# Kernel optimization log

Hardware: AMD Instinct MI355X
Metric: run time of the kernel (lower is better)

## Reference

```python
import jax, jax.numpy as jnp
import numpy as np
from functools import partial

EPS = 1e-6

def rmsnorm(x, w):
    rms = jnp.sqrt(jnp.mean(x * x, axis=-1, keepdims=True) + EPS)
    return x * w / rms

def causal_dwconv(x, w):
    # x: [B, T, D], w: [D, 1, k] depthwise kernel (torch Conv1d layout)
    D = x.shape[-1]
    k = w.shape[-1]
    xt = jnp.transpose(x, (0, 2, 1))  # [B, D, T]
    out = jax.lax.conv_general_dilated(
        xt, w, window_strides=(1,), padding=[(k - 1, 0)],
        dimension_numbers=("NCH", "OIH", "NCH"), feature_group_count=D)
    return jnp.transpose(out, (0, 2, 1))  # [B, T, D]

def setup_inputs() -> dict:
    key = jax.random.key(0)
    B, T, D, F, S = 2, 4096, 1024, 4096, 4096
    ks = jax.random.split(key, 20)
    s = 0.02
    return {
        "x": jax.random.normal(ks[0], (B, T, D), jnp.float32),
        "h_prev": jnp.zeros((B, D), jnp.float32),
        "norm1_w": jnp.ones((D,), jnp.float32),
        "conv3_w": jax.random.normal(ks[1], (D, 1, 3), jnp.float32) * s,
        "conv7_w": jax.random.normal(ks[2], (D, 1, 7), jnp.float32) * s,
        "conv15_w": jax.random.normal(ks[3], (D, 1, 15), jnp.float32) * s,
        "mix_w": jax.random.normal(ks[4], (D, D), jnp.float32) * s,
        "norm2_w": jnp.ones((D,), jnp.float32),
        "Wz_w": jax.random.normal(ks[5], (D, D), jnp.float32) * s,
        "Wz_b": jnp.zeros((D,), jnp.float32),
        "Wh_w": jax.random.normal(ks[6], (D, D), jnp.float32) * s,
        "Wh_b": jnp.zeros((D,), jnp.float32),
        "norm3_w": jnp.ones((D,), jnp.float32),
        "slot_keys": jax.random.normal(ks[7], (S, D), jnp.float32) * s,
        "slot_values": jax.random.normal(ks[8], (S, D), jnp.float32) * s,
        "projq_w": jax.random.normal(ks[9], (D, D), jnp.float32) * s,
        "projout_w": jax.random.normal(ks[10], (D, D), jnp.float32) * s,
        "norm4_w": jnp.ones((D,), jnp.float32),
        "gate_w": jax.random.normal(ks[11], (F, D), jnp.float32) * s,
        "up_w": jax.random.normal(ks[12], (F, D), jnp.float32) * s,
        "down_w": jax.random.normal(ks[13], (D, F), jnp.float32) * s,
    }

def resonance_forward(x, h_prev, norm1_w, conv3_w, conv7_w, conv15_w, mix_w,
                      norm2_w, Wz_w, Wz_b, Wh_w, Wh_b, norm3_w, slot_keys,
                      slot_values, projq_w, projout_w, norm4_w, gate_w, up_w, down_w):
    B, T, D = x.shape
    top_k = 2
    # 1. multi-scale causal conv block
    xn = rmsnorm(x, norm1_w)
    conv = causal_dwconv(xn, conv3_w) + causal_dwconv(xn, conv7_w) + causal_dwconv(xn, conv15_w)
    x = x + conv @ mix_w.T
    # 2. MinGRU: precompute gates, then linear recurrence via scan
    xn = rmsnorm(x, norm2_w)
    z = jax.nn.sigmoid(xn @ Wz_w.T + Wz_b)        # [B, T, D]
    h_tilde = xn @ Wh_w.T + Wh_b                  # [B, T, D]
    def step(h, zh):
        zt, ht = zh
        h = (1.0 - zt) * h + zt * ht
        return h, h
    h_last, hs = jax.lax.scan(step, h_prev,
                              (jnp.swapaxes(z, 0, 1), jnp.swapaxes(h_tilde, 0, 1)))
    x = x + jnp.swapaxes(hs, 0, 1)
    # 3. slot memory with top-k routing
    xn = rmsnorm(x, norm3_w)
    q = xn @ projq_w.T
    scores = (q @ slot_keys.T) / jnp.sqrt(jnp.asarray(D, x.dtype))  # [B, T, S]
    topk_vals, topk_ids = jax.lax.top_k(scores, top_k)              # [B, T, k]
    attn = jax.nn.softmax(topk_vals, axis=-1)
    gathered = slot_values[topk_ids]                                # [B, T, k, D]
    retrieved = jnp.einsum("btk,btkd->btd", attn, gathered)
    x = x + retrieved @ projout_w.T
    # 4. SwiGLU FFN
    xn = rmsnorm(x, norm4_w)
    ff = (jax.nn.silu(xn @ gate_w.T) * (xn @ up_w.T)) @ down_w.T
    x = x + ff
    return x, h_last

def reference(x, h_prev, norm1_w, conv3_w, conv7_w, conv15_w, mix_w, norm2_w,
              Wz_w, Wz_b, Wh_w, Wh_b, norm3_w, slot_keys, slot_values,
              projq_w, projout_w, norm4_w, gate_w, up_w, down_w):
    return resonance_forward(x, h_prev, norm1_w, conv3_w, conv7_w, conv15_w,
                             mix_w, norm2_w, Wz_w, Wz_b, Wh_w, Wh_b, norm3_w,
                             slot_keys, slot_values, projq_w, projout_w,
                             norm4_w, gate_w, up_w, down_w)
```

## Files before the change

### kernel.cpp

```cpp
#include <hip/hip_runtime.h>
#include <hip/hip_bf16.h>
#include <cstdint>

#define BB   2
#define TT   4096
#define DD   1024
#define FF   4096
#define SS   4096
#define MTOK (BB * TT)
#define NCHUNK 32
#define TCHUNK 128

typedef __bf16 bf16x8 __attribute__((ext_vector_type(8)));
typedef float  f32x4  __attribute__((ext_vector_type(4)));
typedef __attribute__((address_space(3))) char lds_char;
typedef __attribute__((address_space(1))) char g_char;

struct CvtArgs {
  const float* src[9];
  __hip_bfloat16* dst[9];
  int off4[10];
  int mode[9];
};

__global__ __launch_bounds__(256) void cvt_all_kernel(CvtArgs a) {
  int g = blockIdx.x * 256 + threadIdx.x;
  if (g >= a.off4[9]) return;
  int s = 0;
  while (g >= a.off4[s + 1]) s++;
  int i = g - a.off4[s];
  float4 v = ((const float4*)a.src[s])[i];
  union { ushort4 u; __hip_bfloat16 h[4]; } p;
  p.h[0] = __float2bfloat16(v.x);
  p.h[1] = __float2bfloat16(v.y);
  p.h[2] = __float2bfloat16(v.z);
  p.h[3] = __float2bfloat16(v.w);
  int di = i;
  int m = a.mode[s];
  if (m) {
    int r = i >> 8, c = i & 255;
    int dr = ((r >> 4) << 5) + (r & 15) + ((m == 2) ? 16 : 0);
    di = (dr << 8) + c;
  }
  ((ushort4*)a.dst[s])[di] = p.u;
}

__global__ void wcomb_kernel(const float* __restrict__ w3, const float* __restrict__ w7,
                             const float* __restrict__ w15, float* __restrict__ wc) {
  int d = blockIdx.x * 256 + threadIdx.x;
  if (d >= DD) return;
  for (int j = 0; j < 16; j++) {
    float v = 0.f;
    if (j < 15) {
      v = w15[d * 15 + (14 - j)];
      if (j < 7) v += w7[d * 7 + (6 - j)];
      if (j < 3) v += w3[d * 3 + (2 - j)];
    }
    wc[d * 16 + j] = v;
  }
}

__global__ __launch_bounds__(256) void rms_kernel(const float* __restrict__ x,
                                                  const float* __restrict__ w,
                                                  __hip_bfloat16* __restrict__ ob) {
  const int row = blockIdx.x;
  const int tid = threadIdx.x;
  float4 v = ((const float4*)(x + (size_t)row * DD))[tid];
  float ss = v.x * v.x + v.y * v.y + v.z * v.z + v.w * v.w;
  for (int off = 32; off > 0; off >>= 1) ss += __shfl_down(ss, off, 64);
  __shared__ float wsum[4];
  if ((tid & 63) == 0) wsum[tid >> 6] = ss;
  __syncthreads();
  float tot = wsum[0] + wsum[1] + wsum[2] + wsum[3];
  float rinv = 1.0f / sqrtf(tot * (1.0f / DD) + 1e-6f);
  float4 wg = ((const float4*)w)[tid];
  union { ushort4 u; __hip_bfloat16 h[4]; } p;
  p.h[0] = __float2bfloat16(v.x * wg.x * rinv);
  p.h[1] = __float2bfloat16(v.y * wg.y * rinv);
  p.h[2] = __float2bfloat16(v.z * wg.z * rinv);
  p.h[3] = __float2bfloat16(v.w * wg.w * rinv);
  ((ushort4*)ob)[(size_t)row * 256 + tid] = p.u;
}

__global__ __launch_bounds__(256) void conv_kernel(const __hip_bfloat16* __restrict__ xn,
                                                   const float* __restrict__ wc,
                                                   __hip_bfloat16* __restrict__ outp) {
  __shared__ float xt[78][64];
  __shared__ float wt[64][15];
  const int b = blockIdx.z, t0 = blockIdx.x * 64, d0 = blockIdx.y * 64;
  const int tid = threadIdx.x;
  const int dl = tid & 63;
  for (int idx = tid; idx < 64 * 15; idx += 256) {
    int d = idx / 15, j = idx % 15;
    wt[d][j] = wc[(d0 + d) * 16 + j];
  }
  for (int r = tid >> 6; r < 78; r += 4) {
    int t = t0 - 14 + r;
    xt[r][dl] = (t >= 0) ? __bfloat162float(xn[((size_t)b * TT + t) * DD + d0 + dl]) : 0.f;
  }
  __syncthreads();
  for (int tl = tid >> 6; tl < 64; tl += 4) {
    float acc = 0.f;
#pragma unroll
    for (int j = 0; j < 15; j++) acc += wt[dl][j] * xt[tl + 14 - j][dl];
    outp[((size_t)b * TT + t0 + tl) * DD + d0 + dl] = __float2bfloat16(acc);
  }
}

template <int EPI, int KSPLIT = 1>
__global__ __launch_bounds__(256, 2) void gemm_bt(
    const __hip_bfloat16* __restrict__ A, const __hip_bfloat16* __restrict__ Bm,
    const int M, const int N, const int K,
    float* __restrict__ outf, __hip_bfloat16* __restrict__ outb,
    const float* __restrict__ bias0, const float* __restrict__ bias1) {
  __shared__ __align__(16) __hip_bfloat16 As[128 * 32];
  __shared__ __align__(16) __hip_bfloat16 Bs[128 * 32];
  const int tid = threadIdx.x;
  const int lane = tid & 63;
  const int wave = tid >> 6;
  const int fm = lane & 15, fq = lane >> 4;

  const int nT = gridDim.x;
  const int lin = blockIdx.y * nT + blockIdx.x;
  const int xcd = lin & 7;
  const int idx_ = lin >> 3;
  const int mq = idx_ / nT;
  const int tileM = (xcd * (gridDim.y >> 3) + mq) * 128;
  const int tileN = (idx_ - mq * nT) * 128;

  const int wm = (wave & 1) * 64, wn = (wave >> 1) * 64;

  f32x4 acc[4][4] = {};

  const int srow = tid >> 2;
  const int scol = (tid & 3) * 8;
  const __hip_bfloat16* gA = A + (size_t)(tileM + srow) * K + scol;
  const __hip_bfloat16* gB = Bm + (size_t)(tileN + srow) * K + scol;
  lds_char* ldsA = (lds_char*)(&As[0]);
  lds_char* ldsB = (lds_char*)(&Bs[0]);
  const int wbyte = wave * 1024;

  const int kPer = K / KSPLIT;
  const int kBeg = (KSPLIT > 1) ? blockIdx.z * kPer : 0;
  for (int k0 = kBeg; k0 < kBeg + kPer; k0 += 32) {
    __syncthreads();
    __builtin_amdgcn_global_load_lds((g_char*)(void*)(gA + k0),                  ldsA + wbyte,        16, 0, 0);
    __builtin_amdgcn_global_load_lds((g_char*)(void*)(gA + k0 + (size_t)64 * K), ldsA + wbyte + 4096, 16, 0, 0);
    __builtin_amdgcn_global_load_lds((g_char*)(void*)(gB + k0),                  ldsB + wbyte,        16, 0, 0);
    __builtin_amdgcn_global_load_lds((g_char*)(void*)(gB + k0 + (size_t)64 * K), ldsB + wbyte + 4096, 16, 0, 0);
    __syncthreads();
    bf16x8 af[4], bfr[4];
#pragma unroll
    for (int i = 0; i < 4; i++) {
      af[i]  = *(const bf16x8*)(As + (wm + i * 16 + fm) * 32 + fq * 8);
      bfr[i] = *(const bf16x8*)(Bs + (wn + i * 16 + fm) * 32 + fq * 8);
    }
#pragma unroll
    for (int i = 0; i < 4; i++)
#pragma unroll
      for (int j = 0; j < 4; j++)
        acc[i][j] = __builtin_amdgcn_mfma_f32_16x16x32_bf16(af[i], bfr[j], acc[i][j], 0, 0, 0);
  }

  if constexpr (EPI == 7) {
#pragma unroll
    for (int i = 0; i < 4; i++) {
#pragma unroll
      for (int j = 0; j < 4; j += 2) {
        const int ffcol = (((tileN + wn + j * 16) >> 5) << 4) + fm;
#pragma unroll
        for (int r = 0; r < 4; r++) {
          const int rw = tileM + wm + i * 16 + fq * 4 + r;
          float g = acc[i][j][r];
          float u = acc[i][j + 1][r];
          float v = g / (1.f + __expf(-g)) * u;
          outb[(size_t)rw * FF + ffcol] = __float2bfloat16(v);
        }
      }
    }
  } else {
#pragma unroll
    for (int i = 0; i < 4; i++) {
#pragma unroll
      for (int j = 0; j < 4; j++) {
        const int c = tileN + wn + j * 16 + fm;
#pragma unroll
        for (int r = 0; r < 4; r++) {
          const int rw = tileM + wm + i * 16 + fq * 4 + r;
          const size_t idx = (size_t)rw * N + c;
          float v = acc[i][j][r];
          if constexpr (EPI == 1) {
            v += (c < DD) ? bias0[c] : bias1[c - DD];
            if (c < DD) v = 1.f / (1.f + __expf(-v));
            outb[idx] = __float2bfloat16(v);
          } else if constexpr (EPI == 2) {
            outb[idx] = __float2bfloat16(v);
          } else if constexpr (EPI == 6) {
            outf[(size_t)blockIdx.z * M * N + idx] = v;
          }
        }
      }
    }
  }
}

template <int EPI>
__global__ __launch_bounds__(256, 4) void gemm_bt64(
    const __hip_bfloat16* __restrict__ A, const __hip_bfloat16* __restrict__ Bm,
    const int M, const int N, const int K,
    const float* __restrict__ resid, float* __restrict__ outf,
    __hip_bfloat16* __restrict__ outb) {
  __shared__ __align__(16) __hip_bfloat16 As[64 * 32];
  __shared__ __align__(16) __hip_bfloat16 Bs[128 * 32];
  const int tid = threadIdx.x;
  const int lane = tid & 63;
  const int wave = tid >> 6;
  const int fm = lane & 15, fq = lane >> 4;

  const int nT = gridDim.x;
  const int lin = blockIdx.y * nT + blockIdx.x;
  const int xcd = lin & 7;
  const int idx_ = lin >> 3;
  const int mq = idx_ / nT;
  const int tileM = (xcd * (gridDim.y >> 3) + mq) * 64;
  const int tileN = (idx_ - mq * nT) * 128;

  const int wm = (wave & 1) * 32, wn = (wave >> 1) * 64;

  f32x4 acc[2][4] = {};

  const int srow = tid >> 2;
  const int scol = (tid & 3) * 8;
  const __hip_bfloat16* gA = A + (size_t)(tileM + srow) * K + scol;
  const __hip_bfloat16* gB = Bm + (size_t)(tileN + srow) * K + scol;
  lds_char* ldsA = (lds_char*)(&As[0]);
  lds_char* ldsB = (lds_char*)(&Bs[0]);
  const int wbyte = wave * 1024;

  for (int k0 = 0; k0 < K; k0 += 32) {
    __syncthreads();
    __builtin_amdgcn_global_load_lds((g_char*)(void*)(gA + k0),                  ldsA + wbyte,        16, 0, 0);
    __builtin_amdgcn_global_load_lds((g_char*)(void*)(gB + k0),                  ldsB + wbyte,        16, 0, 0);
    __builtin_amdgcn_global_load_lds((g_char*)(void*)(gB + k0 + (size_t)64 * K), ldsB + wbyte + 4096, 16, 0, 0);
    __syncthreads();
    bf16x8 af[2], bfr[4];
#pragma unroll
    for (int i = 0; i < 2; i++)
      af[i]  = *(const bf16x8*)(As + (wm + i * 16 + fm) * 32 + fq * 8);
#pragma unroll
    for (int j = 0; j < 4; j++)
      bfr[j] = *(const bf16x8*)(Bs + (wn + j * 16 + fm) * 32 + fq * 8);
#pragma unroll
    for (int i = 0; i < 2; i++)
#pragma unroll
      for (int j = 0; j < 4; j++)
        acc[i][j] = __builtin_amdgcn_mfma_f32_16x16x32_bf16(af[i], bfr[j], acc[i][j], 0, 0, 0);
  }

#pragma unroll
  for (int i = 0; i < 2; i++) {
#pragma unroll
    for (int j = 0; j < 4; j++) {
      const int c = tileN + wn + j * 16 + fm;
#pragma unroll
      for (int r = 0; r < 4; r++) {
        const int rw = tileM + wm + i * 16 + fq * 4 + r;
        const size_t idx = (size_t)rw * N + c;
        float v = acc[i][j][r];
        if constexpr (EPI == 0) {
          outf[idx] = resid[idx] + v;
        } else {
          outb[idx] = __float2bfloat16(v);
        }
      }
    }
  }
}

__global__ __launch_bounds__(256) void reduce_down(const float* __restrict__ P,
                                                   const float* __restrict__ resid,
                                                   float* __restrict__ out) {
  size_t i = (size_t)blockIdx.x * 256 + threadIdx.x;
  float4 a = ((const float4*)P)[i];
  float4 b = ((const float4*)(P + (size_t)MTOK * DD))[i];
  float4 rr = ((const float4*)resid)[i];
  float4 o;
  o.x = rr.x + a.x + b.x; o.y = rr.y + a.y + b.y;
  o.z = rr.z + a.z + b.z; o.w = rr.w + a.w + b.w;
  ((float4*)out)[i] = o;
}

__global__ __launch_bounds__(256) void scan_pass1(const __hip_bfloat16* __restrict__ zht,
                                                  float* __restrict__ cA,
                                                  float* __restrict__ cB) {
  const int b = blockIdx.z, c = blockIdx.y;
  const int d = blockIdx.x * 256 + threadIdx.x;
  const __hip_bfloat16* base = zht + (size_t)b * TT * 2048;
  float A = 1.f, Bc = 0.f;
  const int t0 = c * TCHUNK;
  for (int t = t0; t < t0 + TCHUNK; t++) {
    const __hip_bfloat16* rowp = base + (size_t)t * 2048;
    float z = __bfloat162float(rowp[d]);
    float h = __bfloat162float(rowp[DD + d]);
    float om = 1.f - z;
    A *= om;
    Bc = om * Bc + z * h;
  }
  size_t idx = ((size_t)b * NCHUNK + c) * DD + d;
  cA[idx] = A;
  cB[idx] = Bc;
}

__global__ __launch_bounds__(256) void scan_pass2(const float* __restrict__ hp,
                                                  const float* __restrict__ cA,
                                                  const float* __restrict__ cB,
                                                  float* __restrict__ hstart,
                                                  float* __restrict__ hlast) {
  const int b = blockIdx.y;
  const int d = blockIdx.x * 256 + threadIdx.x;
  float h = hp[b * DD + d];
  for (int c = 0; c < NCHUNK; c++) {
    size_t idx = ((size_t)b * NCHUNK + c) * DD + d;
    hstart[idx] = h;
    h = cA[idx] * h + cB[idx];
  }
  hlast[b * DD + d] = h;
}

__global__ __launch_bounds__(256) void scan_pass3(const __hip_bfloat16* __restrict__ zht,
                                                  const float* __restrict__ hstart,
                                                  float* __restrict__ x) {
  const int b = blockIdx.z, c = blockIdx.y;
  const int d = blockIdx.x * 256 + threadIdx.x;
  const __hip_bfloat16* base = zht + (size_t)b * TT * 2048;
  float h = hstart[((size_t)b * NCHUNK + c) * DD + d];
  const int t0 = c * TCHUNK;
  for (int t = t0; t < t0 + TCHUNK; t++) {
    const __hip_bfloat16* rowp = base + (size_t)t * 2048;
    float z = __bfloat162float(rowp[d]);
    float ht = __bfloat162float(rowp[DD + d]);
    h = (1.f - z) * h + z * ht;
    x[((size_t)b * TT + t) * DD + d] += h;
  }
}

__global__ __launch_bounds__(256) void topk_kernel(const __hip_bfloat16* __restrict__ scores,
                                                   const float* __restrict__ sv,
                                                   __hip_bfloat16* __restrict__ ret) {
  const int row = blockIdx.x;
  const int tid = threadIdx.x;
  const __hip_bfloat16* sr = scores + (size_t)row * SS;
  float v0 = -3.4e38f, v1 = -3.4e38f;
  int i0 = 0x7fffffff, i1 = 0x7fffffff;
#pragma unroll
  for (int it = 0; it < 2; it++) {
    int j0 = (it * 256 + tid) * 8;
    bf16x8 v8 = *(const bf16x8*)(sr + j0);
#pragma unroll
    for (int k = 0; k < 8; k++) {
      float v = (float)v8[k];
      int j = j0 + k;
      if (v > v0) { v1 = v0; i1 = i0; v0 = v; i0 = j; }
      else if (v > v1) { v1 = v; i1 = j; }
    }
  }
#define TKMERGE(w0, j0, w1, j1)                                              \
  {                                                                          \
    if (w0 > v0 || (w0 == v0 && j0 < i0)) {                                  \
      float t0v = v0; int t0i = i0; v0 = w0; i0 = j0;                        \
      if (t0v > w1 || (t0v == w1 && t0i < j1)) { v1 = t0v; i1 = t0i; }       \
      else { v1 = w1; i1 = j1; }                                             \
    } else {                                                                 \
      if (w0 > v1 || (w0 == v1 && j0 < i1)) { v1 = w0; i1 = j0; }            \
    }                                                                        \
  }
  for (int off = 32; off > 0; off >>= 1) {
    float w0 = __shfl_down(v0, off, 64), w1 = __shfl_down(v1, off, 64);
    int   j0 = __shfl_down(i0, off, 64), j1 = __shfl_down(i1, off, 64);
    TKMERGE(w0, j0, w1, j1);
  }
  __shared__ float wv0[4], wv1[4];
  __shared__ int   wi0[4], wi1[4];
  __shared__ float sattn[2];
  __shared__ int   sidx[2];
  if ((tid & 63) == 0) { int w = tid >> 6; wv0[w] = v0; wv1[w] = v1; wi0[w] = i0; wi1[w] = i1; }
  __syncthreads();
  if (tid == 0) {
    v0 = wv0[0]; i0 = wi0[0]; v1 = wv1[0]; i1 = wi1[0];
    for (int w = 1; w < 4; w++) { TKMERGE(wv0[w], wi0[w], wv1[w], wi1[w]); }
    float s0 = v0 * (1.f / 32.f), s1 = v1 * (1.f / 32.f);
    float e = __expf(s1 - s0);
    float denom = 1.f + e;
    sattn[0] = 1.f / denom;
    sattn[1] = e / denom;
    sidx[0] = i0; sidx[1] = i1;
  }
  __syncthreads();
  float a0 = sattn[0], a1 = sattn[1];
  const float4* r0 = (const float4*)(sv + (size_t)sidx[0] * DD);
  const float4* r1 = (const float4*)(sv + (size_t)sidx[1] * DD);
  float4 u = r0[tid], w4 = r1[tid];
  union { ushort4 u; __hip_bfloat16 h[4]; } p;
  p.h[0] = __float2bfloat16(a0 * u.x + a1 * w4.x);
  p.h[1] = __float2bfloat16(a0 * u.y + a1 * w4.y);
  p.h[2] = __float2bfloat16(a0 * u.z + a1 * w4.z);
  p.h[3] = __float2bfloat16(a0 * u.w + a1 * w4.w);
  ((ushort4*)(ret + (size_t)row * DD))[tid] = p.u;
#undef TKMERGE
}

extern "C" void kernel_launch(void* const* d_in, const int* in_sizes, int n_in,
                              void* d_out, int out_size, void* d_ws, size_t ws_size,
                              hipStream_t stream) {
  (void)in_sizes; (void)n_in; (void)out_size; (void)ws_size;
  const float* x_in   = (const float*)d_in[0];
  const float* h_prev = (const float*)d_in[1];
  const float* n1w    = (const float*)d_in[2];
  const float* w3     = (const float*)d_in[3];
  const float* w7     = (const float*)d_in[4];
  const float* w15    = (const float*)d_in[5];
  const float* mixw   = (const float*)d_in[6];
  const float* n2w    = (const float*)d_in[7];
  const float* wzw    = (const float*)d_in[8];
  const float* wzb    = (const float*)d_in[9];
  const float* whw    = (const float*)d_in[10];
  const float* whb    = (const float*)d_in[11];
  const float* n3w    = (const float*)d_in[12];
  const float* slotk  = (const float*)d_in[13];
  const float* slotv  = (const float*)d_in[14];
  const float* pqw    = (const float*)d_in[15];
  const float* pow_   = (const float*)d_in[16];
  const float* n4w    = (const float*)d_in[17];
  const float* gatew  = (const float*)d_in[18];
  const float* upw    = (const float*)d_in[19];
  const float* downw  = (const float*)d_in[20];
  float* out = (float*)d_out;

  char* ws = (char*)d_ws;
  size_t o = 0;
  auto alloc = [&](size_t bytes) {
    size_t r = o;
    o += (bytes + 255) & ~(size_t)255;
    return r;
  };
  __hip_bfloat16* wmix = (__hip_bfloat16*)(ws + alloc((size_t)DD * DD * 2));
  __hip_bfloat16* wzht = (__hip_bfloat16*)(ws + alloc((size_t)2 * DD * DD * 2));
  __hip_bfloat16* wpq  = (__hip_bfloat16*)(ws + alloc((size_t)DD * DD * 2));
  __hip_bfloat16* wsk  = (__hip_bfloat16*)(ws + alloc((size_t)SS * DD * 2));
  __hip_bfloat16* wpo  = (__hip_bfloat16*)(ws + alloc((size_t)DD * DD * 2));
  __hip_bfloat16* wfu  = (__hip_bfloat16*)(ws + alloc((size_t)2 * FF * DD * 2));
  __hip_bfloat16* wd   = (__hip_bfloat16*)(ws + alloc((size_t)DD * FF * 2));
  float* wcomb = (float*)(ws + alloc((size_t)DD * 16 * 4));
  float* xws   = (float*)(ws + alloc((size_t)MTOK * DD * 4));
  __hip_bfloat16* xnb  = (__hip_bfloat16*)(ws + alloc((size_t)MTOK * DD * 2));
  __hip_bfloat16* qb   = (__hip_bfloat16*)(ws + alloc((size_t)MTOK * DD * 2));
  __hip_bfloat16* retr = (__hip_bfloat16*)(ws + alloc((size_t)MTOK * DD * 2));
  float* scanA  = (float*)(ws + alloc((size_t)BB * NCHUNK * DD * 4));
  float* scanB  = (float*)(ws + alloc((size_t)BB * NCHUNK * DD * 4));
  float* hstart = (float*)(ws + alloc((size_t)BB * NCHUNK * DD * 4));
  char* big = ws + alloc((size_t)MTOK * FF * 4);
  __hip_bfloat16* xn1b  = (__hip_bfloat16*)big;
  __hip_bfloat16* convb = (__hip_bfloat16*)(big + (size_t)MTOK * DD * 2);
  __hip_bfloat16* zhtb  = (__hip_bfloat16*)big;
  __hip_bfloat16* scoresb = (__hip_bfloat16*)big;
  __hip_bfloat16* ffin  = (__hip_bfloat16*)big;
  float* Pbuf           = (float*)(big + (size_t)MTOK * FF * 2);

  {
    CvtArgs a;
    const float* srcs[9] = {mixw, wzw, whw, pqw, slotk, pow_, gatew, upw, downw};
    __hip_bfloat16* dsts[9] = {wmix, wzht, wzht + (size_t)DD * DD, wpq, wsk, wpo, wfu, wfu, wd};
    int n4s[9] = {DD * DD / 4, DD * DD / 4, DD * DD / 4, DD * DD / 4, SS * DD / 4,
                  DD * DD / 4, FF * DD / 4, FF * DD / 4, DD * FF / 4};
    int modes[9] = {0, 0, 0, 0, 0, 0, 1, 2, 0};
    int acc_ = 0;
    for (int i = 0; i < 9; i++) {
      a.src[i] = srcs[i]; a.dst[i] = dsts[i]; a.off4[i] = acc_; a.mode[i] = modes[i];
      acc_ += n4s[i];
    }
    a.off4[9] = acc_;
    cvt_all_kernel<<<(acc_ + 255) / 256, 256, 0, stream>>>(a);
  }
  wcomb_kernel<<<DD / 256, 256, 0, stream>>>(w3, w7, w15, wcomb);

  rms_kernel<<<MTOK, 256, 0, stream>>>(x_in, n1w, xn1b);
  conv_kernel<<<dim3(TT / 64, DD / 64, BB), 256, 0, stream>>>(xn1b, wcomb, convb);
  gemm_bt64<0><<<dim3(DD / 128, MTOK / 64), 256, 0, stream>>>(
      convb, wmix, MTOK, DD, DD, x_in, xws, nullptr);

  rms_kernel<<<MTOK, 256, 0, stream>>>(xws, n2w, xnb);
  gemm_bt<1><<<dim3(2048 / 128, MTOK / 128), 256, 0, stream>>>(
      xnb, wzht, MTOK, 2048, DD, nullptr, zhtb, wzb, whb);
  scan_pass1<<<dim3(DD / 256, NCHUNK, BB), 256, 0, stream>>>(zhtb, scanA, scanB);
  scan_pass2<<<dim3(DD / 256, BB), 256, 0, stream>>>(h_prev, scanA, scanB, hstart,
                                                     out + (size_t)MTOK * DD);
  scan_pass3<<<dim3(DD / 256, NCHUNK, BB), 256, 0, stream>>>(zhtb, hstart, xws);

  rms_kernel<<<MTOK, 256, 0, stream>>>(xws, n3w, xnb);
  gemm_bt64<2><<<dim3(DD / 128, MTOK / 64), 256, 0, stream>>>(
      xnb, wpq, MTOK, DD, DD, nullptr, nullptr, qb);
  gemm_bt<2><<<dim3(SS / 128, MTOK / 128), 256, 0, stream>>>(
      qb, wsk, MTOK, SS, DD, nullptr, scoresb, nullptr, nullptr);
  topk_kernel<<<MTOK, 256, 0, stream>>>(scoresb, slotv, retr);
  gemm_bt64<0><<<dim3(DD / 128, MTOK / 64), 256, 0, stream>>>(
      retr, wpo, MTOK, DD, DD, xws, xws, nullptr);

  rms_kernel<<<MTOK, 256, 0, stream>>>(xws, n4w, xnb);
  gemm_bt<7><<<dim3(2 * FF / 128, MTOK / 128), 256, 0, stream>>>(
      xnb, wfu, MTOK, 2 * FF, DD, nullptr, ffin, nullptr, nullptr);
  gemm_bt<6, 2><<<dim3(DD / 128, MTOK / 128, 2), 256, 0, stream>>>(
      ffin, wd, MTOK, DD, FF, Pbuf, nullptr, nullptr, nullptr);
  reduce_down<<<MTOK * DD / 1024, 256, 0, stream>>>(Pbuf, xws, out);
}
```

Measured before the change: 791.3 us.

## Fuse per-tile top-2 selection into score GEMM epilogue; add N-major tile swizzle

The slot-score GEMM no longer writes the full bf16 score matrix. Its epilogue now reduces each 128-column tile to top-2 candidates per row through lane shuffles and LDS, then stores one float4 per row per tile. A new light merge kernel combines the 32 candidates per row and does the weighted gather of slot values. This removes the write and re-read of a large score buffer. Separately, a new block swizzle that assigns N-tiles to XCDs is applied to the zh and gate/up GEMMs, changing cache locality; scores are now kept in fp32 instead of bf16, which may alter tie behaviour slightly.

New measurement: 813.7 us. 2.8% more time.

```diff
diff --git a/kernel.cpp b/kernel.cpp
--- a/kernel.cpp
+++ b/kernel.cpp
@@ -1,6 +1,8 @@
 #include <hip/hip_runtime.h>
 #include <hip/hip_bf16.h>
 #include <cstdint>
+#include <cfloat>
+#include <climits>
 
 #define BB   2
 #define TT   4096
@@ -15,6 +17,17 @@
 typedef float  f32x4  __attribute__((ext_vector_type(4)));
 typedef __attribute__((address_space(3))) char lds_char;
 typedef __attribute__((address_space(1))) char g_char;
+
+#define TKMERGE(w0, j0, w1, j1)                                              \
+  {                                                                          \
+    if (w0 > v0 || (w0 == v0 && j0 < i0)) {                                  \
+      float t0v = v0; int t0i = i0; v0 = w0; i0 = j0;                        \
+      if (t0v > w1 || (t0v == w1 && t0i < j1)) { v1 = t0v; i1 = t0i; }       \
+      else { v1 = w1; i1 = j1; }                                             \
+    } else {                                                                 \
+      if (w0 > v1 || (w0 == v1 && j0 < i1)) { v1 = w0; i1 = j0; }            \
+    }                                                                        \
+  }
 
 struct CvtArgs {
   const float* src[9];
@@ -107,7 +120,7 @@
   }
 }
 
-template <int EPI, int KSPLIT = 1>
+template <int EPI, int KSPLIT = 1, int SWZ = 0>
 __global__ __launch_bounds__(256, 2) void gemm_bt(
     const __hip_bfloat16* __restrict__ A, const __hip_bfloat16* __restrict__ Bm,
     const int M, const int N, const int K,
@@ -122,11 +135,22 @@
 
   const int nT = gridDim.x;
   const int lin = blockIdx.y * nT + blockIdx.x;
-  const int xcd = lin & 7;
-  const int idx_ = lin >> 3;
-  const int mq = idx_ / nT;
-  const int tileM = (xcd * (gridDim.y >> 3) + mq) * 128;
-  const int tileN = (idx_ - mq * nT) * 128;
+  int tileM, tileN;
+  if constexpr (SWZ == 0) {
+    const int xcd = lin & 7;
+    const int idx_ = lin >> 3;
+    const int mq = idx_ / nT;
+    tileM = (xcd * (gridDim.y >> 3) + mq) * 128;
+    tileN = (idx_ - mq * nT) * 128;
+  } else {
+    const int xcd = lin & 7;
+    const int idx_ = lin >> 3;
+    const int nS = nT >> 3;
+    const int m = idx_ / nS;
+    const int nl = idx_ - m * nS;
+    tileM = m * 128;
+    tileN = (xcd * nS + nl) * 128;
+  }
 
   const int wm = (wave & 1) * 64, wn = (wave >> 1) * 64;
 
@@ -175,6 +199,70 @@
           float u = acc[i][j + 1][r];
           float v = g / (1.f + __expf(-g)) * u;
           outb[(size_t)rw * FF + ffcol] = __float2bfloat16(v);
+        }
+      }
+    }
+  } else if constexpr (EPI == 8) {
+    __syncthreads();
+    __shared__ float lv[128][2];
+    __shared__ int   li[128][2];
+#pragma unroll
+    for (int i = 0; i < 4; i++) {
+#pragma unroll
+      for (int r = 0; r < 4; r++) {
+        float v0 = -FLT_MAX, v1 = -FLT_MAX;
+        int i0 = INT_MAX, i1 = INT_MAX;
+#pragma unroll
+        for (int j = 0; j < 4; j++) {
+          float v = acc[i][j][r];
+          int c = tileN + wn + j * 16 + fm;
+          if (v > v0) { v1 = v0; i1 = i0; v0 = v; i0 = c; }
+          else if (v > v1) { v1 = v; i1 = c; }
+        }
+#pragma unroll
+        for (int off = 1; off < 16; off <<= 1) {
+          float w0 = __shfl_xor(v0, off, 64), w1 = __shfl_xor(v1, off, 64);
+          int   j0 = __shfl_xor(i0, off, 64), j1 = __shfl_xor(i1, off, 64);
+          TKMERGE(w0, j0, w1, j1);
+        }
+        const int lrow = wm + i * 16 + fq * 4 + r;
+        if (wn == 64 && fm == 0) {
+          lv[lrow][0] = v0; lv[lrow][1] = v1;
+          li[lrow][0] = i0; li[lrow][1] = i1;
+        }
+      }
+    }
+    __syncthreads();
+    if (wn == 0) {
+#pragma unroll
+      for (int i = 0; i < 4; i++) {
+#pragma unroll
+        for (int r = 0; r < 4; r++) {
+          float v0 = -FLT_MAX, v1 = -FLT_MAX;
+          int i0 = INT_MAX, i1 = INT_MAX;
+#pragma unroll
+          for (int j = 0; j < 4; j++) {
+            float v = acc[i][j][r];
+            int c = tileN + wn + j * 16 + fm;
+            if (v > v0) { v1 = v0; i1 = i0; v0 = v; i0 = c; }
+            else if (v > v1) { v1 = v; i1 = c; }
+          }
+#pragma unroll
+          for (int off = 1; off < 16; off <<= 1) {
+            float w0 = __shfl_xor(v0, off, 64), w1 = __shfl_xor(v1, off, 64);
+            int   j0 = __shfl_xor(i0, off, 64), j1 = __shfl_xor(i1, off, 64);
+            TKMERGE(w0, j0, w1, j1);
+          }
+          const int lrow = wm + i * 16 + fq * 4 + r;
+          if (fm == 0) {
+            float w0 = lv[lrow][0], w1 = lv[lrow][1];
+            int   j0 = li[lrow][0], j1 = li[lrow][1];
+            TKMERGE(w0, j0, w1, j1);
+            float4 c4;
+            c4.x = v0; c4.y = v1;
+            c4.z = __int_as_float(i0); c4.w = __int_as_float(i1);
+            ((float4*)outf)[(size_t)(tileM + lrow) * (SS / 128) + (tileN >> 7)] = c4;
+          }
         }
       }
     }
@@ -344,69 +432,42 @@
   }
 }
 
-__global__ __launch_bounds__(256) void topk_kernel(const __hip_bfloat16* __restrict__ scores,
-                                                   const float* __restrict__ sv,
-                                                   __hip_bfloat16* __restrict__ ret) {
-  const int row = blockIdx.x;
-  const int tid = threadIdx.x;
-  const __hip_bfloat16* sr = scores + (size_t)row * SS;
-  float v0 = -3.4e38f, v1 = -3.4e38f;
-  int i0 = 0x7fffffff, i1 = 0x7fffffff;
-#pragma unroll
-  for (int it = 0; it < 2; it++) {
-    int j0 = (it * 256 + tid) * 8;
-    bf16x8 v8 = *(const bf16x8*)(sr + j0);
-#pragma unroll
-    for (int k = 0; k < 8; k++) {
-      float v = (float)v8[k];
-      int j = j0 + k;
-      if (v > v0) { v1 = v0; i1 = i0; v0 = v; i0 = j; }
-      else if (v > v1) { v1 = v; i1 = j; }
-    }
-  }
-#define TKMERGE(w0, j0, w1, j1)                                              \
-  {                                                                          \
-    if (w0 > v0 || (w0 == v0 && j0 < i0)) {                                  \
-      float t0v = v0; int t0i = i0; v0 = w0; i0 = j0;                        \
-      if (t0v > w1 || (t0v == w1 && t0i < j1)) { v1 = t0v; i1 = t0i; }       \
-      else { v1 = w1; i1 = j1; }                                             \
-    } else {                                                                 \
-      if (w0 > v1 || (w0 == v1 && j0 < i1)) { v1 = w0; i1 = j0; }            \
-    }                                                                        \
-  }
-  for (int off = 32; off > 0; off >>= 1) {
-    float w0 = __shfl_down(v0, off, 64), w1 = __shfl_down(v1, off, 64);
-    int   j0 = __shfl_down(i0, off, 64), j1 = __shfl_down(i1, off, 64);
+__global__ __launch_bounds__(256) void topk_merge(const float4* __restrict__ cand,
+                                                  const float* __restrict__ sv,
+                                                  __hip_bfloat16* __restrict__ ret) {
+  const int row = blockIdx.x * 4 + (threadIdx.x >> 6);
+  const int lane = threadIdx.x & 63;
+  float v0 = -FLT_MAX, v1 = -FLT_MAX;
+  int i0 = INT_MAX, i1 = INT_MAX;
+  if (lane < 32) {
+    float4 c = cand[(size_t)row * 32 + lane];
+    v0 = c.x; v1 = c.y;
+    i0 = __float_as_int(c.z); i1 = __float_as_int(c.w);
+  }
+#pragma unroll
+  for (int off = 1; off < 64; off <<= 1) {
+    float w0 = __shfl_xor(v0, off, 64), w1 = __shfl_xor(v1, off, 64);
+    int   j0 = __shfl_xor(i0, off, 64), j1 = __shfl_xor(i1, off, 64);
     TKMERGE(w0, j0, w1, j1);
   }
-  __shared__ float wv0[4], wv1[4];
-  __shared__ int   wi0[4], wi1[4];
-  __shared__ float sattn[2];
-  __shared__ int   sidx[2];
-  if ((tid & 63) == 0) { int w = tid >> 6; wv0[w] = v0; wv1[w] = v1; wi0[w] = i0; wi1[w] = i1; }
-  __syncthreads();
-  if (tid == 0) {
-    v0 = wv0[0]; i0 = wi0[0]; v1 = wv1[0]; i1 = wi1[0];
-    for (int w = 1; w < 4; w++) { TKMERGE(wv0[w], wi0[w], wv1[w], wi1[w]); }
-    float s0 = v0 * (1.f / 32.f), s1 = v1 * (1.f / 32.f);
-    float e = __expf(s1 - s0);
-    float denom = 1.f + e;
-    sattn[0] = 1.f / denom;
-    sattn[1] = e / denom;
-    sidx[0] = i0; sidx[1] = i1;
-  }
-  __syncthreads();
-  float a0 = sattn[0], a1 = sattn[1];
-  const float4* r0 = (const float4*)(sv + (size_t)sidx[0] * DD);
-  const float4* r1 = (const float4*)(sv + (size_t)sidx[1] * DD);
-  float4 u = r0[tid], w4 = r1[tid];
-  union { ushort4 u; __hip_bfloat16 h[4]; } p;
-  p.h[0] = __float2bfloat16(a0 * u.x + a1 * w4.x);
-  p.h[1] = __float2bfloat16(a0 * u.y + a1 * w4.y);
-  p.h[2] = __float2bfloat16(a0 * u.z + a1 * w4.z);
-  p.h[3] = __float2bfloat16(a0 * u.w + a1 * w4.w);
-  ((ushort4*)(ret + (size_t)row * DD))[tid] = p.u;
-#undef TKMERGE
+  float s0 = v0 * (1.f / 32.f), s1 = v1 * (1.f / 32.f);
+  float e = __expf(s1 - s0);
+  float denom = 1.f + e;
+  float a0 = 1.f / denom;
+  float a1 = e / denom;
+  const float4* r0 = (const float4*)(sv + (size_t)i0 * DD);
+  const float4* r1 = (const float4*)(sv + (size_t)i1 * DD);
+#pragma unroll
+  for (int k = 0; k < 4; k++) {
+    int j = lane + 64 * k;
+    float4 u = r0[j], w4 = r1[j];
+    union { ushort4 u; __hip_bfloat16 h[4]; } p;
+    p.h[0] = __float2bfloat16(a0 * u.x + a1 * w4.x);
+    p.h[1] = __float2bfloat16(a0 * u.y + a1 * w4.y);
+    p.h[2] = __float2bfloat16(a0 * u.z + a1 * w4.z);
+    p.h[3] = __float2bfloat16(a0 * u.w + a1 * w4.w);
+    ((ushort4*)(ret + (size_t)row * DD))[j] = p.u;
+  }
 }
 
 extern "C" void kernel_launch(void* const* d_in, const int* in_sizes, int n_in,
@@ -462,7 +523,7 @@
   __hip_bfloat16* xn1b  = (__hip_bfloat16*)big;
   __hip_bfloat16* convb = (__hip_bfloat16*)(big + (size_t)MTOK * DD * 2);
   __hip_bfloat16* zhtb  = (__hip_bfloat16*)big;
-  __hip_bfloat16* scoresb = (__hip_bfloat16*)big;
+  float* candf          = (float*)big;
   __hip_bfloat16* ffin  = (__hip_bfloat16*)big;
   float* Pbuf           = (float*)(big + (size_t)MTOK * FF * 2);
 
@@ -489,7 +550,7 @@
       convb, wmix, MTOK, DD, DD, x_in, xws, nullptr);
 
   rms_kernel<<<MTOK, 256, 0, stream>>>(xws, n2w, xnb);
-  gemm_bt<1><<<dim3(2048 / 128, MTOK / 128), 256, 0, stream>>>(
+  gemm_bt<1, 1, 1><<<dim3(2048 / 128, MTOK / 128), 256, 0, stream>>>(
       xnb, wzht, MTOK, 2048, DD, nullptr, zhtb, wzb, whb);
   scan_pass1<<<dim3(DD / 256, NCHUNK, BB), 256, 0, stream>>>(zhtb, scanA, scanB);
   scan_pass2<<<dim3(DD / 256, BB), 256, 0, stream>>>(h_prev, scanA, scanB, hstart,
@@ -499,16 +560,16 @@
   rms_kernel<<<MTOK, 256, 0, stream>>>(xws, n3w, xnb);
   gemm_bt64<2><<<dim3(DD / 128, MTOK / 64), 256, 0, stream>>>(
       xnb, wpq, MTOK, DD, DD, nullptr, nullptr, qb);
-  gemm_bt<2><<<dim3(SS / 128, MTOK / 128), 256, 0, stream>>>(
-      qb, wsk, MTOK, SS, DD, nullptr, scoresb, nullptr, nullptr);
-  topk_kernel<<<MTOK, 256, 0, stream>>>(scoresb, slotv, retr);
+  gemm_bt<8, 1, 1><<<dim3(SS / 128, MTOK / 128), 256, 0, stream>>>(
+      qb, wsk, MTOK, SS, DD, candf, nullptr, nullptr, nullptr);
+  topk_merge<<<MTOK / 4, 256, 0, stream>>>((const float4*)candf, slotv, retr);
   gemm_bt64<0><<<dim3(DD / 128, MTOK / 64), 256, 0, stream>>>(
       retr, wpo, MTOK, DD, DD, xws, xws, nullptr);
 
   rms_kernel<<<MTOK, 256, 0, stream>>>(xws, n4w, xnb);
-  gemm_bt<7><<<dim3(2 * FF / 128, MTOK / 128), 256, 0, stream>>>(
+  gemm_bt<7, 1, 1><<<dim3(2 * FF / 128, MTOK / 128), 256, 0, stream>>>(
       xnb, wfu, MTOK, 2 * FF, DD, nullptr, ffin, nullptr, nullptr);
-  gemm_bt<6, 2><<<dim3(DD / 128, MTOK / 128, 2), 256, 0, stream>>>(
+  gemm_bt<6, 2, 0><<<dim3(DD / 128, MTOK / 128, 2), 256, 0, stream>>>(
       ffin, wd, MTOK, DD, FF, Pbuf, nullptr, nullptr, nullptr);
   reduce_down<<<MTOK * DD / 1024, 256, 0, stream>>>(Pbuf, xws, out);
 }
```
